# Kernel tuning notes

Measured on AMD Instinct MI355X. Metric: run time of the kernel, lower is better.

## Reference

```python
import jax, jax.numpy as jnp
import numpy as np
from jax import lax

N = 100000   # input points
M = 100000   # output points
CIN = 64
COUT = 64
K = 3        # cubic kernel size
G = 50       # grid side (points live at voxel centers of a G^3 grid)
SHIFT = 1    # coordinate shift so border queries (coord -1) stay non-negative
B = 64       # per-axis encode base, > G + K; key fits easily in int32


def _encode(c):
    # c: [..., 3] int32 xyz voxel coords -> unique int32 key
    c = c + SHIFT
    return (c[..., 2] * B + c[..., 1]) * B + c[..., 0]


def setup_inputs() -> dict:
    rng = np.random.RandomState(0)
    total = G ** 3

    def decode(idx):
        x = idx % G
        y = (idx // G) % G
        z = idx // (G * G)
        # +0.5 moves points to voxel centers (as in the layer's docstring example)
        return np.stack([x, y, z], axis=1).astype(np.float32) + 0.5

    inp_positions = jnp.asarray(decode(rng.permutation(total)[:N]))
    out_positions = jnp.asarray(decode(rng.permutation(total)[:M]))

    key = jax.random.key(0)
    k1, k2 = jax.random.split(key, 2)
    inp_features = jax.random.normal(k1, (N, CIN), jnp.float32)
    kernel = jax.random.normal(k2, (K, K, K, CIN, COUT), jnp.float32) * 0.05
    bias = jnp.zeros((COUT,), jnp.float32)
    voxel_size = jnp.ones((), jnp.float32)
    return {
        "inp_features": inp_features,
        "inp_positions": inp_positions,
        "out_positions": out_positions,
        "voxel_size": voxel_size,
        "kernel": kernel,
        "bias": bias,
    }


def reference(inp_features, inp_positions, out_positions, voxel_size, kernel, bias):
    # SparseConv on a regular grid: odd cubic kernel -> offset = 0, Linf radius
    # K*voxel*0.51 selects exactly the K^3 voxel neighborhood. Nearest-neighbor
    # interpolation with identity mapping maps relative offset d in [-r, r]^3
    # to filter tap index d + r on each axis (x = width = last spatial dim).
    inp_coord = jnp.floor(inp_positions / voxel_size).astype(jnp.int32)  # [N,3]
    out_coord = jnp.floor(out_positions / voxel_size).astype(jnp.int32)  # [M,3]

    # sorted-key hash table over input voxels
    keys = _encode(inp_coord)                    # [N]
    order = jnp.argsort(keys)
    skeys = keys[order]
    feats = inp_features[order]                  # [N, Cin]

    r = K // 2
    K3 = K ** 3
    ks = jnp.arange(K3)
    # flat kernel order is (z, y, x) to match kernel.reshape(K3, Cin, Cout)
    d_xyz = jnp.stack([ks % K - r, (ks // K) % K - r, ks // (K * K) - r],
                      axis=1).astype(jnp.int32)  # [K3, 3]
    Kmat = kernel.reshape(K3, CIN, COUT)

    n_inp = skeys.shape[0]

    def step(acc, xs):
        d, W = xs                                 # d: [3], W: [Cin, Cout]
        qk = _encode(out_coord + d)               # [M]
        p = jnp.searchsorted(skeys, qk)
        pc = jnp.clip(p, 0, n_inp - 1)
        found = (skeys[pc] == qk)[:, None]        # [M, 1]
        g = jnp.where(found, feats[pc], 0.0)      # [M, Cin]
        return acc + g @ W, None

    out0 = jnp.zeros((out_coord.shape[0], COUT), inp_features.dtype)
    out, _ = lax.scan(step, out0, (d_xyz, Kmat))
    return out + bias
```

## Files before the change

kernel.cpp:

```cpp
#include <hip/hip_runtime.h>
#include <math.h>

#define GY 54
#define NROWS (54*54*64)

#define HX 10
#define HY 6
#define HXY 60
#define NH 360
#define NBX 7
#define NBY 13
#define NBRICK (7*13*13)
#define SLAB 148

#define LDK 72

typedef __bf16  bf16x8 __attribute__((ext_vector_type(8)));
typedef float  f32x16 __attribute__((ext_vector_type(16)));

__global__ void prep_kernel(const float* __restrict__ ipos, int n,
                            const float* __restrict__ opos, int m,
                            const float* __restrict__ vsp,
                            const float* __restrict__ W,
                            int* __restrict__ imap, int* __restrict__ ikey,
                            int* __restrict__ omap, int* __restrict__ okey,
                            __bf16* __restrict__ Wt) {
    int i = blockIdx.x * 256 + threadIdx.x;
    float vs = vsp[0];
    if (i < n) {
        int x = (int)floorf(ipos[3*i+0] / vs) + 1;
        int y = (int)floorf(ipos[3*i+1] / vs) + 1;
        int z = (int)floorf(ipos[3*i+2] / vs) + 1;
        int key = (z * GY + y) * 64 + x;
        ikey[i] = key;
        imap[key] = i;
    } else if (i < n + m) {
        int j = i - n;
        int x = (int)floorf(opos[3*j+0] / vs) + 1;
        int y = (int)floorf(opos[3*j+1] / vs) + 1;
        int z = (int)floorf(opos[3*j+2] / vs) + 1;
        int key = (z * GY + y) * 64 + x;
        okey[j] = key;
        omap[key] = j;
    } else if (i < n + m + 27*64*64) {
        int k  = i - n - m;
        int t  = k >> 12;
        int r  = k & 4095;
        int ci = r >> 6;
        int co = r & 63;
        Wt[(t << 12) + (co << 6) + ci] = (__bf16)W[k];
    }
}

__global__ __launch_bounds__(256, 2) void conv_kernel(
    const float* __restrict__ feats,
    const __bf16* __restrict__ Wt,
    const float* __restrict__ bias,
    const int*   __restrict__ imap,
    const int*   __restrict__ ikey,
    const int*   __restrict__ omap,
    const int*   __restrict__ okey,
    float*       __restrict__ out,
    int N, int M)
{
    __shared__ __align__(16) __bf16 halo[NH * LDK];
    __shared__ __align__(16) __bf16 Bld[2][64 * LDK];
    __shared__ int ridx[NH];
    __shared__ int obuf[128];

    const int tid = threadIdx.x;

    int q = (blockIdx.x & 7) * SLAB + (blockIdx.x >> 3);
    if (q >= NBRICK) return;
    const int bx = q % NBX;
    int rem = q / NBX;
    const int by = rem % NBY;
    const int bz = rem / NBY;

    const int wr0 = tid >> 3;
    const int wr1 = 32 + wr0;
    const int wc  = tid & 7;

    float4 wreg0 = *(const float4*)(Wt + wr0 * 64 + wc * 8);
    float4 wreg1 = *(const float4*)(Wt + wr1 * 64 + wc * 8);
    *(float4*)(&Bld[0][wr0 * LDK + wc * 8]) = wreg0;
    *(float4*)(&Bld[0][wr1 * LDK + wc * 8]) = wreg1;
    wreg0 = *(const float4*)(Wt + 4096 + wr0 * 64 + wc * 8);
    wreg1 = *(const float4*)(Wt + 4096 + wr1 * 64 + wc * 8);

    #pragma unroll
    for (int it = 0; it < 2; ++it) {
        int r = it * 256 + tid;
        if (r < NH) {
            int xs = r % HX;
            int t2 = r / HX;
            int ys = t2 % HY;
            int zs = t2 / HY;
            int key = ((bz*4 + zs) * GY + (by*4 + ys)) * 64 + (bx*8 + xs);
            int idx = imap[key];
            int c = min(max(idx, 0), N - 1);
            ridx[r] = (idx >= 0 && idx < N && ikey[c] == key) ? idx : -1;
        }
    }
    if (tid < 128) {
        int x = tid & 7, y = (tid >> 3) & 3, z = tid >> 5;
        int key = ((bz*4 + z + 1) * GY + (by*4 + y + 1)) * 64 + (bx*8 + x + 1);
        int o = omap[key];
        int c = min(max(o, 0), M - 1);
        obuf[tid] = (o >= 0 && o < M && okey[c] == key) ? o : -1;
    }
    __syncthreads();

    #pragma unroll
    for (int it = 0; it < 12; ++it) {
        int task = it * 256 + tid;
        if (task < NH * 8) {
            int r = task >> 3, c = task & 7;
            int idx = ridx[r];
            bf16x8 v;
            if (idx >= 0) {
                const float4* s = (const float4*)(feats + (size_t)idx * 64 + c * 8);
                float4 f0 = s[0], f1 = s[1];
                v[0]=(__bf16)f0.x; v[1]=(__bf16)f0.y; v[2]=(__bf16)f0.z; v[3]=(__bf16)f0.w;
                v[4]=(__bf16)f1.x; v[5]=(__bf16)f1.y; v[6]=(__bf16)f1.z; v[7]=(__bf16)f1.w;
            } else {
                #pragma unroll
                for (int j = 0; j < 8; ++j) v[j] = (__bf16)0.f;
            }
            *(bf16x8*)(halo + r * LDK + c * 8) = v;
        }
    }

    const int wave  = tid >> 6;
    const int lane  = tid & 63;
    const int lrow  = lane & 31;
    const int halfk = lane >> 5;
    const int xv = lrow & 7, yv = (lrow >> 3) & 3;
    const __bf16* Abase = halo + ((wave + 1) * HXY + (yv + 1) * HX + (xv + 1)) * LDK
                               + halfk * 8;
    const int Bb0 = lrow * LDK + halfk * 8;
    const int Bb1 = Bb0 + 32 * LDK;

    f32x16 acc0, acc1;
    #pragma unroll
    for (int i = 0; i < 16; ++i) { acc0[i] = 0.f; acc1[i] = 0.f; }

    __syncthreads();

    bf16x8 acur[4];
    {
        const __bf16* Ab = Abase + (-1 * HXY - 1 * HX - 1) * LDK;
        #pragma unroll
        for (int kc = 0; kc < 4; ++kc) acur[kc] = *(const bf16x8*)(Ab + kc * 16);
    }

    #pragma unroll
    for (int t = 0; t < 27; ++t) {
        if (t < 26) {
            __bf16* nb = &Bld[(t + 1) & 1][0];
            *(float4*)(nb + wr0 * LDK + wc * 8) = wreg0;
            *(float4*)(nb + wr1 * LDK + wc * 8) = wreg1;
        }
        if (t < 25) {
            const __bf16* wp = Wt + ((size_t)(t + 2) << 12);
            wreg0 = *(const float4*)(wp + wr0 * 64 + wc * 8);
            wreg1 = *(const float4*)(wp + wr1 * 64 + wc * 8);
        }

        const __bf16* Bbuf = &Bld[t & 1][0];
        bf16x8 b0[4], b1[4];
        #pragma unroll
        for (int kc = 0; kc < 4; ++kc) {
            b0[kc] = *(const bf16x8*)(Bbuf + Bb0 + kc * 16);
            b1[kc] = *(const bf16x8*)(Bbuf + Bb1 + kc * 16);
        }

        bf16x8 anext[4];
        if (t < 26) {
            const int tn = t + 1;
            const int dx = tn % 3 - 1;
            const int dy = (tn / 3) % 3 - 1;
            const int dz = tn / 9 - 1;
            const __bf16* An = Abase + (dz * HXY + dy * HX + dx) * LDK;
            #pragma unroll
            for (int kc = 0; kc < 4; ++kc) anext[kc] = *(const bf16x8*)(An + kc * 16);
        }

        #pragma unroll
        for (int kc = 0; kc < 4; ++kc) {
            acc0 = __builtin_amdgcn_mfma_f32_32x32x16_bf16(acur[kc], b0[kc], acc0, 0, 0, 0);
            acc1 = __builtin_amdgcn_mfma_f32_32x32x16_bf16(acur[kc], b1[kc], acc1, 0, 0, 0);
        }

        if (t < 26) {
            #pragma unroll
            for (int kc = 0; kc < 4; ++kc) acur[kc] = anext[kc];
        }
        __syncthreads();
    }

    const int col0 = lrow, col1 = 32 + lrow;
    const float bv0 = bias[col0], bv1 = bias[col1];
    #pragma unroll
    for (int r = 0; r < 16; ++r) {
        int mrow = (r & 3) + 8 * (r >> 2) + 4 * halfk;
        int orow = obuf[wave * 32 + mrow];
        if (orow >= 0) {
            out[(size_t)orow * 64 + col0] = acc0[r] + bv0;
            out[(size_t)orow * 64 + col1] = acc1[r] + bv1;
        }
    }
}

extern "C" void kernel_launch(void* const* d_in, const int* in_sizes, int n_in,
                              void* d_out, int out_size, void* d_ws, size_t ws_size,
                              hipStream_t stream) {
    const float* feats = (const float*)d_in[0];
    const float* ipos  = (const float*)d_in[1];
    const float* opos  = (const float*)d_in[2];
    const float* vsp   = (const float*)d_in[3];
    const float* W     = (const float*)d_in[4];
    const float* bias  = (const float*)d_in[5];

    int N = in_sizes[0] / 64;
    int M = out_size / 64;

    int*    imap = (int*)d_ws;
    int*    omap = imap + NROWS;
    int*    ikey = omap + NROWS;
    int*    okey = ikey + N;
    __bf16* Wt   = (__bf16*)(okey + M);

    int total = N + M + 27*64*64;
    prep_kernel<<<(total + 255) / 256, 256, 0, stream>>>(ipos, N, opos, M, vsp, W,
                                                         imap, ikey, omap, okey, Wt);
    conv_kernel<<<8 * SLAB, 256, 0, stream>>>(feats, Wt, bias, imap, ikey, omap, okey,
                                              (float*)d_out, N, M);
}
```

Baseline: 145.1 us.

## Load weights directly from global into registers and drop per-tap barriers

The shared-memory double buffer for per-tap weight matrices is removed. Each lane now loads its MFMA B fragments straight from global/L2 into registers, with two taps of prefetch, so the 27 per-tap __syncthreads disappear. The neighbor-index lookup is fused into the halo gather, removing the ridx shared array and one barrier. This trades LDS traffic and synchronisation for more global loads per wave, since weights are fetched redundantly by all four waves, and for higher register pressure from the double-buffered A and B fragments.

```diff
diff --git a/kernel.cpp b/kernel.cpp
--- a/kernel.cpp
+++ b/kernel.cpp
@@ -64,8 +64,6 @@
     int N, int M)
 {
     __shared__ __align__(16) __bf16 halo[NH * LDK];
-    __shared__ __align__(16) __bf16 Bld[2][64 * LDK];
-    __shared__ int ridx[NH];
     __shared__ int obuf[128];
 
     const int tid = threadIdx.x;
@@ -77,48 +75,36 @@
     const int by = rem % NBY;
     const int bz = rem / NBY;
 
-    const int wr0 = tid >> 3;
-    const int wr1 = 32 + wr0;
-    const int wc  = tid & 7;
-
-    float4 wreg0 = *(const float4*)(Wt + wr0 * 64 + wc * 8);
-    float4 wreg1 = *(const float4*)(Wt + wr1 * 64 + wc * 8);
-    *(float4*)(&Bld[0][wr0 * LDK + wc * 8]) = wreg0;
-    *(float4*)(&Bld[0][wr1 * LDK + wc * 8]) = wreg1;
-    wreg0 = *(const float4*)(Wt + 4096 + wr0 * 64 + wc * 8);
-    wreg1 = *(const float4*)(Wt + 4096 + wr1 * 64 + wc * 8);
-
-    #pragma unroll
-    for (int it = 0; it < 2; ++it) {
-        int r = it * 256 + tid;
-        if (r < NH) {
+    const int wave  = tid >> 6;
+    const int lane  = tid & 63;
+    const int lrow  = lane & 31;
+    const int halfk = lane >> 5;
+
+    const __bf16* Wl = Wt + lrow * 64 + halfk * 8;
+    bf16x8 Bp0[8], Bp1[8];
+    #pragma unroll
+    for (int kc = 0; kc < 4; ++kc) {
+        Bp0[kc]     = *(const bf16x8*)(Wl + kc * 16);
+        Bp0[4 + kc] = *(const bf16x8*)(Wl + 2048 + kc * 16);
+        Bp1[kc]     = *(const bf16x8*)(Wl + 4096 + kc * 16);
+        Bp1[4 + kc] = *(const bf16x8*)(Wl + 4096 + 2048 + kc * 16);
+    }
+
+    #pragma unroll
+    for (int it = 0; it < 12; ++it) {
+        int task = it * 256 + tid;
+        if (task < NH * 8) {
+            int r = task >> 3, c = task & 7;
             int xs = r % HX;
             int t2 = r / HX;
             int ys = t2 % HY;
             int zs = t2 / HY;
             int key = ((bz*4 + zs) * GY + (by*4 + ys)) * 64 + (bx*8 + xs);
             int idx = imap[key];
-            int c = min(max(idx, 0), N - 1);
-            ridx[r] = (idx >= 0 && idx < N && ikey[c] == key) ? idx : -1;
-        }
-    }
-    if (tid < 128) {
-        int x = tid & 7, y = (tid >> 3) & 3, z = tid >> 5;
-        int key = ((bz*4 + z + 1) * GY + (by*4 + y + 1)) * 64 + (bx*8 + x + 1);
-        int o = omap[key];
-        int c = min(max(o, 0), M - 1);
-        obuf[tid] = (o >= 0 && o < M && okey[c] == key) ? o : -1;
-    }
-    __syncthreads();
-
-    #pragma unroll
-    for (int it = 0; it < 12; ++it) {
-        int task = it * 256 + tid;
-        if (task < NH * 8) {
-            int r = task >> 3, c = task & 7;
-            int idx = ridx[r];
+            int cl  = min(max(idx, 0), N - 1);
+            bool ok = (idx >= 0 && idx < N && ikey[cl] == key);
             bf16x8 v;
-            if (idx >= 0) {
+            if (ok) {
                 const float4* s = (const float4*)(feats + (size_t)idx * 64 + c * 8);
                 float4 f0 = s[0], f1 = s[1];
                 v[0]=(__bf16)f0.x; v[1]=(__bf16)f0.y; v[2]=(__bf16)f0.z; v[3]=(__bf16)f0.w;
@@ -130,16 +116,17 @@
             *(bf16x8*)(halo + r * LDK + c * 8) = v;
         }
     }
-
-    const int wave  = tid >> 6;
-    const int lane  = tid & 63;
-    const int lrow  = lane & 31;
-    const int halfk = lane >> 5;
+    if (tid < 128) {
+        int x = tid & 7, y = (tid >> 3) & 3, z = tid >> 5;
+        int key = ((bz*4 + z + 1) * GY + (by*4 + y + 1)) * 64 + (bx*8 + x + 1);
+        int o = omap[key];
+        int cl = min(max(o, 0), M - 1);
+        obuf[tid] = (o >= 0 && o < M && okey[cl] == key) ? o : -1;
+    }
+
     const int xv = lrow & 7, yv = (lrow >> 3) & 3;
     const __bf16* Abase = halo + ((wave + 1) * HXY + (yv + 1) * HX + (xv + 1)) * LDK
                                + halfk * 8;
-    const int Bb0 = lrow * LDK + halfk * 8;
-    const int Bb1 = Bb0 + 32 * LDK;
 
     f32x16 acc0, acc1;
     #pragma unroll
@@ -147,56 +134,54 @@
 
     __syncthreads();
 
-    bf16x8 acur[4];
+    bf16x8 Ap0[4], Ap1[4];
     {
-        const __bf16* Ab = Abase + (-1 * HXY - 1 * HX - 1) * LDK;
-        #pragma unroll
-        for (int kc = 0; kc < 4; ++kc) acur[kc] = *(const bf16x8*)(Ab + kc * 16);
+        const __bf16* a0 = Abase + (-1 * HXY - 1 * HX - 1) * LDK;
+        const __bf16* a1 = Abase + (-1 * HXY - 1 * HX + 0) * LDK;
+        #pragma unroll
+        for (int kc = 0; kc < 4; ++kc) {
+            Ap0[kc] = *(const bf16x8*)(a0 + kc * 16);
+            Ap1[kc] = *(const bf16x8*)(a1 + kc * 16);
+        }
     }
 
     #pragma unroll
     for (int t = 0; t < 27; ++t) {
-        if (t < 26) {
-            __bf16* nb = &Bld[(t + 1) & 1][0];
-            *(float4*)(nb + wr0 * LDK + wc * 8) = wreg0;
-            *(float4*)(nb + wr1 * LDK + wc * 8) = wreg1;
-        }
+        bf16x8 a[4], b[8];
+        #pragma unroll
+        for (int kc = 0; kc < 4; ++kc) a[kc] = (t & 1) ? Ap1[kc] : Ap0[kc];
+        #pragma unroll
+        for (int j = 0; j < 8; ++j)   b[j]  = (t & 1) ? Bp1[j]  : Bp0[j];
+
         if (t < 25) {
-            const __bf16* wp = Wt + ((size_t)(t + 2) << 12);
-            wreg0 = *(const float4*)(wp + wr0 * 64 + wc * 8);
-            wreg1 = *(const float4*)(wp + wr1 * 64 + wc * 8);
-        }
-
-        const __bf16* Bbuf = &Bld[t & 1][0];
-        bf16x8 b0[4], b1[4];
-        #pragma unroll
-        for (int kc = 0; kc < 4; ++kc) {
-            b0[kc] = *(const bf16x8*)(Bbuf + Bb0 + kc * 16);
-            b1[kc] = *(const bf16x8*)(Bbuf + Bb1 + kc * 16);
-        }
-
-        bf16x8 anext[4];
-        if (t < 26) {
-            const int tn = t + 1;
+            const int tn = t + 2;
+            const __bf16* wp = Wl + ((size_t)tn << 12);
             const int dx = tn % 3 - 1;
             const int dy = (tn / 3) % 3 - 1;
             const int dz = tn / 9 - 1;
-            const __bf16* An = Abase + (dz * HXY + dy * HX + dx) * LDK;
-            #pragma unroll
-            for (int kc = 0; kc < 4; ++kc) anext[kc] = *(const bf16x8*)(An + kc * 16);
+            const __bf16* an = Abase + (dz * HXY + dy * HX + dx) * LDK;
+            if (t & 1) {
+                #pragma unroll
+                for (int kc = 0; kc < 4; ++kc) {
+                    Bp1[kc]     = *(const bf16x8*)(wp + kc * 16);
+                    Bp1[4 + kc] = *(const bf16x8*)(wp + 2048 + kc * 16);
+                    Ap1[kc]     = *(const bf16x8*)(an + kc * 16);
+                }
+            } else {
+                #pragma unroll
+                for (int kc = 0; kc < 4; ++kc) {
+                    Bp0[kc]     = *(const bf16x8*)(wp + kc * 16);
+                    Bp0[4 + kc] = *(const bf16x8*)(wp + 2048 + kc * 16);
+                    Ap0[kc]     = *(const bf16x8*)(an + kc * 16);
+                }
+            }
         }
 
         #pragma unroll
         for (int kc = 0; kc < 4; ++kc) {
-            acc0 = __builtin_amdgcn_mfma_f32_32x32x16_bf16(acur[kc], b0[kc], acc0, 0, 0, 0);
-            acc1 = __builtin_amdgcn_mfma_f32_32x32x16_bf16(acur[kc], b1[kc], acc1, 0, 0, 0);
-        }
-
-        if (t < 26) {
-            #pragma unroll
-            for (int kc = 0; kc < 4; ++kc) acur[kc] = anext[kc];
-        }
-        __syncthreads();
+            acc0 = __builtin_amdgcn_mfma_f32_32x32x16_bf16(a[kc], b[kc],     acc0, 0, 0, 0);
+            acc1 = __builtin_amdgcn_mfma_f32_32x32x16_bf16(a[kc], b[4 + kc], acc1, 0, 0, 0);
+        }
     }
 
     const int col0 = lrow, col1 = 32 + lrow;
```

New measurement: 245.4 us. +69.1%, slower.

## Split input channels into two halves to shrink LDS and raise occupancy

Applied to the files above, without the earlier changes.

Splits the 64 input channels into two 32-channel passes. Each pass gathers half of every halo row into LDS and runs the 27-tap MFMA loop over a matching half-width weight slab, which prep now writes in a per-half layout. The LDS footprint per block roughly halves, so launch bounds go from 2 to 4 blocks per CU to hide gather latency better. In exchange the tap loop and its barriers run twice, and the halo gather becomes two serialized phases per block.

```diff
diff --git a/kernel.cpp b/kernel.cpp
--- a/kernel.cpp
+++ b/kernel.cpp
@@ -13,7 +13,7 @@
 #define NBRICK (7*13*13)
 #define SLAB 148
 
-#define LDK 72
+#define LDH 36
 
 typedef __bf16  bf16x8 __attribute__((ext_vector_type(8)));
 typedef float  f32x16 __attribute__((ext_vector_type(16)));
@@ -24,7 +24,7 @@
                             const float* __restrict__ W,
                             int* __restrict__ imap, int* __restrict__ ikey,
                             int* __restrict__ omap, int* __restrict__ okey,
-                            __bf16* __restrict__ Wt) {
+                            __bf16* __restrict__ Wt2) {
     int i = blockIdx.x * 256 + threadIdx.x;
     float vs = vsp[0];
     if (i < n) {
@@ -48,13 +48,15 @@
         int r  = k & 4095;
         int ci = r >> 6;
         int co = r & 63;
-        Wt[(t << 12) + (co << 6) + ci] = (__bf16)W[k];
+        int h   = ci >> 5;
+        int cil = ci & 31;
+        Wt2[(((h * 27 + t) << 6) + co) * 32 + cil] = (__bf16)W[k];
     }
 }
 
-__global__ __launch_bounds__(256, 2) void conv_kernel(
+__global__ __launch_bounds__(256, 4) void conv_kernel(
     const float* __restrict__ feats,
-    const __bf16* __restrict__ Wt,
+    const __bf16* __restrict__ Wt2,
     const float* __restrict__ bias,
     const int*   __restrict__ imap,
     const int*   __restrict__ ikey,
@@ -63,8 +65,8 @@
     float*       __restrict__ out,
     int N, int M)
 {
-    __shared__ __align__(16) __bf16 halo[NH * LDK];
-    __shared__ __align__(16) __bf16 Bld[2][64 * LDK];
+    __shared__ __align__(16) __bf16 halo[NH * LDH];
+    __shared__ __align__(16) __bf16 Bld[2][64 * LDH];
     __shared__ int ridx[NH];
     __shared__ int obuf[128];
 
@@ -76,17 +78,6 @@
     int rem = q / NBX;
     const int by = rem % NBY;
     const int bz = rem / NBY;
-
-    const int wr0 = tid >> 3;
-    const int wr1 = 32 + wr0;
-    const int wc  = tid & 7;
-
-    float4 wreg0 = *(const float4*)(Wt + wr0 * 64 + wc * 8);
-    float4 wreg1 = *(const float4*)(Wt + wr1 * 64 + wc * 8);
-    *(float4*)(&Bld[0][wr0 * LDK + wc * 8]) = wreg0;
-    *(float4*)(&Bld[0][wr1 * LDK + wc * 8]) = wreg1;
-    wreg0 = *(const float4*)(Wt + 4096 + wr0 * 64 + wc * 8);
-    wreg1 = *(const float4*)(Wt + 4096 + wr1 * 64 + wc * 8);
 
     #pragma unroll
     for (int it = 0; it < 2; ++it) {
@@ -109,37 +100,19 @@
         int c = min(max(o, 0), M - 1);
         obuf[tid] = (o >= 0 && o < M && okey[c] == key) ? o : -1;
     }
-    __syncthreads();
-
-    #pragma unroll
-    for (int it = 0; it < 12; ++it) {
-        int task = it * 256 + tid;
-        if (task < NH * 8) {
-            int r = task >> 3, c = task & 7;
-            int idx = ridx[r];
-            bf16x8 v;
-            if (idx >= 0) {
-                const float4* s = (const float4*)(feats + (size_t)idx * 64 + c * 8);
-                float4 f0 = s[0], f1 = s[1];
-                v[0]=(__bf16)f0.x; v[1]=(__bf16)f0.y; v[2]=(__bf16)f0.z; v[3]=(__bf16)f0.w;
-                v[4]=(__bf16)f1.x; v[5]=(__bf16)f1.y; v[6]=(__bf16)f1.z; v[7]=(__bf16)f1.w;
-            } else {
-                #pragma unroll
-                for (int j = 0; j < 8; ++j) v[j] = (__bf16)0.f;
-            }
-            *(bf16x8*)(halo + r * LDK + c * 8) = v;
-        }
-    }
 
     const int wave  = tid >> 6;
     const int lane  = tid & 63;
     const int lrow  = lane & 31;
     const int halfk = lane >> 5;
     const int xv = lrow & 7, yv = (lrow >> 3) & 3;
-    const __bf16* Abase = halo + ((wave + 1) * HXY + (yv + 1) * HX + (xv + 1)) * LDK
+    const __bf16* Abase = halo + ((wave + 1) * HXY + (yv + 1) * HX + (xv + 1)) * LDH
                                + halfk * 8;
-    const int Bb0 = lrow * LDK + halfk * 8;
-    const int Bb1 = Bb0 + 32 * LDK;
+    const int Bb0 = lrow * LDH + halfk * 8;
+    const int Bb1 = Bb0 + 32 * LDH;
+
+    const int wr = tid >> 2;
+    const int wc = tid & 3;
 
     f32x16 acc0, acc1;
     #pragma unroll
@@ -147,56 +120,75 @@
 
     __syncthreads();
 
-    bf16x8 acur[4];
-    {
-        const __bf16* Ab = Abase + (-1 * HXY - 1 * HX - 1) * LDK;
+    for (int h = 0; h < 2; ++h) {
         #pragma unroll
-        for (int kc = 0; kc < 4; ++kc) acur[kc] = *(const bf16x8*)(Ab + kc * 16);
-    }
-
-    #pragma unroll
-    for (int t = 0; t < 27; ++t) {
-        if (t < 26) {
-            __bf16* nb = &Bld[(t + 1) & 1][0];
-            *(float4*)(nb + wr0 * LDK + wc * 8) = wreg0;
-            *(float4*)(nb + wr1 * LDK + wc * 8) = wreg1;
-        }
-        if (t < 25) {
-            const __bf16* wp = Wt + ((size_t)(t + 2) << 12);
-            wreg0 = *(const float4*)(wp + wr0 * 64 + wc * 8);
-            wreg1 = *(const float4*)(wp + wr1 * 64 + wc * 8);
-        }
-
-        const __bf16* Bbuf = &Bld[t & 1][0];
-        bf16x8 b0[4], b1[4];
+        for (int it = 0; it < 6; ++it) {
+            int task = it * 256 + tid;
+            if (task < NH * 4) {
+                int r = task >> 2, c = task & 3;
+                int idx = ridx[r];
+                bf16x8 v;
+                if (idx >= 0) {
+                    const float4* s = (const float4*)(feats + (size_t)idx * 64 + h * 32 + c * 8);
+                    float4 f0 = s[0], f1 = s[1];
+                    v[0]=(__bf16)f0.x; v[1]=(__bf16)f0.y; v[2]=(__bf16)f0.z; v[3]=(__bf16)f0.w;
+                    v[4]=(__bf16)f1.x; v[5]=(__bf16)f1.y; v[6]=(__bf16)f1.z; v[7]=(__bf16)f1.w;
+                } else {
+                    #pragma unroll
+                    for (int j = 0; j < 8; ++j) v[j] = (__bf16)0.f;
+                }
+                *(bf16x8*)(halo + r * LDH + c * 8) = v;
+            }
+        }
+
+        const __bf16* Wh = Wt2 + h * 27 * 2048;
+        float4 wreg = *(const float4*)(Wh + wr * 32 + wc * 8);
+        *(float4*)(&Bld[0][wr * LDH + wc * 8]) = wreg;
+        wreg = *(const float4*)(Wh + 2048 + wr * 32 + wc * 8);
+
+        __syncthreads();
+
+        bf16x8 acur0, acur1;
+        {
+            const __bf16* Ab = Abase + (-HXY - HX - 1) * LDH;
+            acur0 = *(const bf16x8*)(Ab);
+            acur1 = *(const bf16x8*)(Ab + 16);
+        }
+
         #pragma unroll
-        for (int kc = 0; kc < 4; ++kc) {
-            b0[kc] = *(const bf16x8*)(Bbuf + Bb0 + kc * 16);
-            b1[kc] = *(const bf16x8*)(Bbuf + Bb1 + kc * 16);
-        }
-
-        bf16x8 anext[4];
-        if (t < 26) {
-            const int tn = t + 1;
-            const int dx = tn % 3 - 1;
-            const int dy = (tn / 3) % 3 - 1;
-            const int dz = tn / 9 - 1;
-            const __bf16* An = Abase + (dz * HXY + dy * HX + dx) * LDK;
-            #pragma unroll
-            for (int kc = 0; kc < 4; ++kc) anext[kc] = *(const bf16x8*)(An + kc * 16);
-        }
-
-        #pragma unroll
-        for (int kc = 0; kc < 4; ++kc) {
-            acc0 = __builtin_amdgcn_mfma_f32_32x32x16_bf16(acur[kc], b0[kc], acc0, 0, 0, 0);
-            acc1 = __builtin_amdgcn_mfma_f32_32x32x16_bf16(acur[kc], b1[kc], acc1, 0, 0, 0);
-        }
-
-        if (t < 26) {
-            #pragma unroll
-            for (int kc = 0; kc < 4; ++kc) acur[kc] = anext[kc];
-        }
-        __syncthreads();
+        for (int t = 0; t < 27; ++t) {
+            if (t < 26) {
+                *(float4*)(&Bld[(t + 1) & 1][wr * LDH + wc * 8]) = wreg;
+            }
+            if (t < 25) {
+                wreg = *(const float4*)(Wh + (t + 2) * 2048 + wr * 32 + wc * 8);
+            }
+
+            const __bf16* Bbuf = &Bld[t & 1][0];
+            bf16x8 b00 = *(const bf16x8*)(Bbuf + Bb0);
+            bf16x8 b01 = *(const bf16x8*)(Bbuf + Bb0 + 16);
+            bf16x8 b10 = *(const bf16x8*)(Bbuf + Bb1);
+            bf16x8 b11 = *(const bf16x8*)(Bbuf + Bb1 + 16);
+
+            bf16x8 an0, an1;
+            if (t < 26) {
+                const int tn = t + 1;
+                const int dx = tn % 3 - 1;
+                const int dy = (tn / 3) % 3 - 1;
+                const int dz = tn / 9 - 1;
+                const __bf16* An = Abase + (dz * HXY + dy * HX + dx) * LDH;
+                an0 = *(const bf16x8*)(An);
+                an1 = *(const bf16x8*)(An + 16);
+            }
+
+            acc0 = __builtin_amdgcn_mfma_f32_32x32x16_bf16(acur0, b00, acc0, 0, 0, 0);
+            acc1 = __builtin_amdgcn_mfma_f32_32x32x16_bf16(acur0, b10, acc1, 0, 0, 0);
+            acc0 = __builtin_amdgcn_mfma_f32_32x32x16_bf16(acur1, b01, acc0, 0, 0, 0);
+            acc1 = __builtin_amdgcn_mfma_f32_32x32x16_bf16(acur1, b11, acc1, 0, 0, 0);
+
+            if (t < 26) { acur0 = an0; acur1 = an1; }
+            __syncthreads();
+        }
     }
 
     const int col0 = lrow, col1 = 32 + lrow;
@@ -229,11 +221,11 @@
     int*    omap = imap + NROWS;
     int*    ikey = omap + NROWS;
     int*    okey = ikey + N;
-    __bf16* Wt   = (__bf16*)(okey + M);
+    __bf16* Wt2  = (__bf16*)(okey + M);
 
     int total = N + M + 27*64*64;
     prep_kernel<<<(total + 255) / 256, 256, 0, stream>>>(ipos, N, opos, M, vsp, W,
-                                                         imap, ikey, omap, okey, Wt);
-    conv_kernel<<<8 * SLAB, 256, 0, stream>>>(feats, Wt, bias, imap, ikey, omap, okey,
+                                                         imap, ikey, omap, okey, Wt2);
+    conv_kernel<<<8 * SLAB, 256, 0, stream>>>(feats, Wt2, bias, imap, ikey, omap, okey,
                                               (float*)d_out, N, M);
 }
```

After: 275.3 us. 1.9x slower.
